# Kernel optimization log

Measured on AMD Instinct MI355X. Metric: run time of the kernel, lower is better.

## Reference

```python
import jax, jax.numpy as jnp
import numpy as np

B, N, E = 32, 1024, 16384
IN_DIM, HID, OUT = 768, 512, 400
H, F = 2, 200          # gat heads, per-head dim (H*F == OUT)
PAIR = 2 * OUT         # 800
NEG_SLOPE = 0.2


def setup_inputs() -> dict:
    key = jax.random.key(0)
    ks = jax.random.split(key, 20)
    g = lambda k, shp, fan: jax.random.normal(k, shp, jnp.float32) * (1.0 / np.sqrt(fan))
    return {
        "patch_features": jax.random.normal(ks[0], (B, N, IN_DIM), jnp.float32),
        "edges": jax.random.randint(ks[1], (2, E), 0, N, jnp.int32),
        # patch_encoder Mlps: 768 -> 512 (GELU) -> 400
        "enc_w1": g(ks[2], (IN_DIM, HID), IN_DIM), "enc_b1": jnp.zeros((HID,), jnp.float32),
        "enc_w2": g(ks[3], (HID, OUT), HID),      "enc_b2": jnp.zeros((OUT,), jnp.float32),
        # single GATConv: 400 -> 2 heads x 200, concat
        "gat_w": g(ks[4], (OUT, H, F), OUT),
        "att_src": g(ks[5], (H, F), F), "att_dst": g(ks[6], (H, F), F),
        "gat_b": jnp.zeros((H * F,), jnp.float32),
        # predict_head Mlps: 800 -> 800 (GELU) -> 400 (GELU) -> 3
        "h_w1": g(ks[7], (PAIR, PAIR), PAIR),      "h_b1": jnp.zeros((PAIR,), jnp.float32),
        "h_w2": g(ks[8], (PAIR, PAIR // 2), PAIR), "h_b2": jnp.zeros((PAIR // 2,), jnp.float32),
        "h_w3": g(ks[9], (PAIR // 2, 3), PAIR // 2), "h_b3": jnp.zeros((3,), jnp.float32),
    }


def _forward(patch_features, edges, enc_w1, enc_b1, enc_w2, enc_b2,
             gat_w, att_src, att_dst, gat_b,
             h_w1, h_b1, h_w2, h_b2, h_w3, h_b3):
    n = patch_features.shape[1]
    # per-batch patch encoder MLP (dropout inactive at eval)
    enc = jax.nn.gelu(jnp.einsum('bni,ih->bnh', patch_features, enc_w1) + enc_b1)
    enc = jnp.einsum('bnh,ho->bno', enc, enc_w2) + enc_b2   # [B,N,400]

    src0, dst0 = edges[0], edges[1]
    # GATConv adds self-loops
    loops = jnp.arange(n, dtype=edges.dtype)
    src = jnp.concatenate([src0, loops])
    dst = jnp.concatenate([dst0, loops])

    def gat(h):                                   # h: [N,400]
        wh = jnp.einsum('no,ohf->nhf', h, gat_w)  # [N,H,F]
        a_s = jnp.sum(wh * att_src, -1)           # [N,H]
        a_d = jnp.sum(wh * att_dst, -1)
        e = a_s[src] + a_d[dst]                   # [Et,H]
        e = jnp.where(e > 0, e, NEG_SLOPE * e)    # LeakyReLU(0.2)
        m = jax.ops.segment_max(e, dst, num_segments=n)
        ee = jnp.exp(e - m[dst])
        z = jax.ops.segment_sum(ee, dst, num_segments=n)
        coef = ee / z[dst]                        # softmax over incoming edges
        out = jax.ops.segment_sum(coef[:, :, None] * wh[src], dst, num_segments=n)
        return out.reshape(n, H * F) + gat_b      # concat heads + bias

    feat = enc + jax.vmap(gat)(enc)               # residual add per batch

    # pairwise edge gather + predict head
    pair = jnp.concatenate([feat[:, src0], feat[:, dst0]], axis=-1)  # [B,E,800]
    p = jax.nn.gelu(jnp.einsum('bep,pq->beq', pair, h_w1) + h_b1)
    p = jax.nn.gelu(jnp.einsum('beq,qr->ber', p, h_w2) + h_b2)
    pred = jnp.einsum('ber,rs->bes', p, h_w3) + h_b3                 # [B,E,3]
    return feat, pred


def reference(patch_features, edges, enc_w1, enc_b1, enc_w2, enc_b2,
              gat_w, att_src, att_dst, gat_b,
              h_w1, h_b1, h_w2, h_b2, h_w3, h_b3):
    return _forward(patch_features, edges, enc_w1, enc_b1, enc_w2, enc_b2,
                    gat_w, att_src, att_dst, gat_b,
                    h_w1, h_b1, h_w2, h_b2, h_w3, h_b3)
```

## Files before the change

### kernel.cpp

```cpp
#include <hip/hip_runtime.h>
#include <hip/hip_bf16.h>

typedef unsigned short u16;
typedef __attribute__((ext_vector_type(8))) short bf16x8;
typedef __attribute__((ext_vector_type(4))) float f32x4;

#define B_   32
#define N_   1024
#define E_   16384
#define ET_  17408
#define IN_DIM 768
#define HID  512
#define OUT_ 400
#define PAIR_ 800
#define UVW_ 1600
#define FEAT_ELEMS 13107200
#define MAXD 128

__device__ __forceinline__ float u2f(u16 u) {
    union { unsigned int i; float f; } v; v.i = ((unsigned int)u) << 16; return v.f;
}
__device__ __forceinline__ u16 f2u(float f) {
    __hip_bfloat16 h = __float2bfloat16(f);
    return *(u16*)&h;
}
__device__ __forceinline__ unsigned int pack2(float a, float b) {
    return (unsigned int)f2u(a) | ((unsigned int)f2u(b) << 16);
}

__device__ __forceinline__ float gelu_f(float x) {
    const float c = 0.7978845608028654f;
    float u = c * (x + 0.044715f * x * x * x);
    float t = 2.0f / (1.0f + __expf(-2.0f * u)) - 1.0f;
    return 0.5f * x * (1.0f + t);
}

__device__ __forceinline__ void load_lds16(const void* g, void* l) {
    __builtin_amdgcn_global_load_lds(
        (const __attribute__((address_space(1))) void*)g,
        (__attribute__((address_space(3))) void*)l, 16, 0, 0);
}

__global__ void wt_k(const float* __restrict__ W, u16* __restrict__ Wt,
                     int K, int N)
{
    int i = blockIdx.x * 256 + threadIdx.x;
    if (i >= N * K) return;
    int n = i / K, k = i - n * K;
    Wt[i] = f2u(W[(size_t)k * N + n]);
}

__global__ void wtuv_k(const float* __restrict__ W, u16* __restrict__ Wt)
{
    int i = blockIdx.x * 256 + threadIdx.x;
    if (i >= UVW_ * OUT_) return;
    int n = i / OUT_, k = i - n * OUT_;
    int row = (n >= PAIR_) ? OUT_ + k : k;
    int col = (n >= PAIR_) ? n - PAIR_ : n;
    Wt[i] = f2u(W[(size_t)row * PAIR_ + col]);
}

__global__ void f2b_k(const float* __restrict__ X, u16* __restrict__ Y, int n8)
{
    int i = blockIdx.x * 256 + threadIdx.x;
    if (i >= n8) return;
    const float4* p = (const float4*)X + (size_t)i * 2;
    float4 a = p[0], b = p[1];
    uint4 o;
    o.x = pack2(a.x, a.y); o.y = pack2(a.z, a.w);
    o.z = pack2(b.x, b.y); o.w = pack2(b.z, b.w);
    ((uint4*)Y)[i] = o;
}

template<int ASRC, bool DO_GELU, bool HAS_BIAS, bool OUT_F32, bool FUSE_H3, bool WIDE>
__global__ __launch_bounds__(WIDE ? 512 : 256, 2)
void mfma_gemm_k(const float* __restrict__ Af, const u16* __restrict__ Ab,
                 const u16* __restrict__ Wt, const float* __restrict__ bias,
                 u16* __restrict__ Cb, float* __restrict__ Cf,
                 int M, int N, int K,
                 const u16* __restrict__ zbuf,
                 const float* __restrict__ w3p, float* __restrict__ partp)
{
    static_assert(!WIDE || ASRC == 1, "wide path requires bf16 async staging");
    constexpr int BM  = WIDE ? 256 : 128;
    constexpr int BN  = WIDE ? 256 : 128;
    constexpr int NWV = WIDE ? 8 : 4;
    constexpr int UN  = WIDE ? 8 : 4;
    constexpr int WNS = WIDE ? 128 : 64;

    __shared__ __align__(16) u16 As[2][BM * 64];
    __shared__ __align__(16) u16 Bs[2][BN * 64];
    const int tid  = threadIdx.x;
    const int gx   = gridDim.x;
    const int nwg  = gx * gridDim.y;
    const int orig = blockIdx.y * gx + blockIdx.x;
    const int qc   = nwg >> 3, rc = nwg & 7;
    const int xcd  = orig & 7, lid = orig >> 3;
    const int wg   = ((xcd < rc) ? xcd * (qc + 1) : rc * (qc + 1) + (xcd - rc) * qc) + lid;
    const int bnIdx= wg % gx;
    const int bm   = (wg / gx) * BM;
    const int bn   = bnIdx * BN;
    const int wave = tid >> 6;
    const int lane = tid & 63;
    const int wm   = (wave >> 1) * 64;
    const int wn   = (wave & 1) * WNS;
    const int lm   = lane & 15;
    const int lq   = lane >> 4;
    const int lb   = lm & 7;
    const int l8 = lane >> 3;
    const int cl = (lane & 7) ^ l8;

    size_t arow[4]; size_t brow[4]; bool bok[4];
    #pragma unroll
    for (int c4 = 0; c4 < 4; ++c4) {
        int rt = wave * 32 + c4 * 8 + l8;
        if (ASRC == 1) arow[c4] = (size_t)(bm + rt) * K;
        int n = bn + rt;
        bok[c4] = (n < N);
        brow[c4] = (size_t)(n < N ? n : 0) * K;
    }
    const int vrow = tid >> 1, vhalf = tid & 1;

    f32x4 acc[4][UN] = {};
    const int NT = (K + 63) >> 6;

    if (ASRC == 1) {
        auto stage = [&](int buf, int k0) {
            int kk = k0 + cl * 8;
            #pragma unroll
            for (int c4 = 0; c4 < 4; ++c4) {
                const u16* ga = (kk < K) ? Ab + arow[c4] + kk : zbuf;
                load_lds16(ga, (char*)As[buf] + (wave * 32 + c4 * 8) * 128);
            }
            #pragma unroll
            for (int c4 = 0; c4 < 4; ++c4) {
                const u16* gb = (bok[c4] && kk < K) ? Wt + brow[c4] + kk : zbuf;
                load_lds16(gb, (char*)Bs[buf] + (wave * 32 + c4 * 8) * 128);
            }
        };
        stage(0, 0);
        int cur = 0;
        for (int it = 0; it < NT; ++it) {
            const bool last = (it == NT - 1);
            if (!last) stage(cur ^ 1, (it + 1) * 64);
            if (!last) asm volatile("s_waitcnt vmcnt(8)" ::: "memory");
            else       asm volatile("s_waitcnt vmcnt(0)" ::: "memory");
            __builtin_amdgcn_s_barrier();
            const char* Abase = (const char*)As[cur];
            const char* Bbase = (const char*)Bs[cur];
            #pragma unroll
            for (int kh = 0; kh < 2; ++kh) {
                bf16x8 af[4], bfr[UN];
                #pragma unroll
                for (int t = 0; t < 4; ++t)
                    af[t] = *(const bf16x8*)(Abase +
                            (wm + t * 16 + lm) * 128 + (((kh * 4 + lq) ^ lb) * 16));
                #pragma unroll
                for (int u = 0; u < UN; ++u)
                    bfr[u] = *(const bf16x8*)(Bbase +
                            (wn + u * 16 + lm) * 128 + (((kh * 4 + lq) ^ lb) * 16));
                #pragma unroll
                for (int t = 0; t < 4; ++t)
                    #pragma unroll
                    for (int u = 0; u < UN; ++u)
                        acc[t][u] = __builtin_amdgcn_mfma_f32_16x16x32_bf16(
                            af[t], bfr[u], acc[t][u], 0, 0, 0);
            }
            asm volatile("" ::: "memory");
            __builtin_amdgcn_s_barrier();
            cur ^= 1;
        }
    } else {
        for (int k0 = 0; k0 < K; k0 += 64) {
            #pragma unroll
            for (int c = 0; c < 4; ++c) {
                int c_log = vhalf * 4 + c;
                int kk = k0 + c_log * 8;
                uint4 wv = make_uint4(0, 0, 0, 0);
                if (kk < K) {
                    const float* p = Af + (size_t)(bm + vrow) * K + kk;
                    float4 v0 = *(const float4*)p;
                    float4 v1 = *(const float4*)(p + 4);
                    wv.x = pack2(v0.x, v0.y); wv.y = pack2(v0.z, v0.w);
                    wv.z = pack2(v1.x, v1.y); wv.w = pack2(v1.z, v1.w);
                }
                int pc = c_log ^ (vrow & 7);
                *(uint4*)((char*)As[0] + vrow * 128 + pc * 16) = wv;
            }
            {
                int kk = k0 + cl * 8;
                #pragma unroll
                for (int c4 = 0; c4 < 4; ++c4) {
                    const u16* gb = (bok[c4] && kk < K) ? Wt + brow[c4] + kk : zbuf;
                    load_lds16(gb, (char*)Bs[0] + (wave * 32 + c4 * 8) * 128);
                }
            }
            __syncthreads();
            #pragma unroll
            for (int kh = 0; kh < 2; ++kh) {
                bf16x8 af[4], bfr[UN];
                #pragma unroll
                for (int t = 0; t < 4; ++t)
                    af[t] = *(const bf16x8*)((const char*)As[0] +
                            (wm + t * 16 + lm) * 128 + (((kh * 4 + lq) ^ lb) * 16));
                #pragma unroll
                for (int u = 0; u < UN; ++u)
                    bfr[u] = *(const bf16x8*)((const char*)Bs[0] +
                            (wn + u * 16 + lm) * 128 + (((kh * 4 + lq) ^ lb) * 16));
                #pragma unroll
                for (int t = 0; t < 4; ++t)
                    #pragma unroll
                    for (int u = 0; u < UN; ++u)
                        acc[t][u] = __builtin_amdgcn_mfma_f32_16x16x32_bf16(
                            af[t], bfr[u], acc[t][u], 0, 0, 0);
            }
            __syncthreads();
        }
    }

    if (FUSE_H3) {
        float w3c[UN][3]; float bvv[UN];
        #pragma unroll
        for (int u = 0; u < UN; ++u) {
            int col = bn + wn + u * 16 + lm;
            bool ok = (col < N);
            bvv[u]    = ok ? bias[col] : 0.f;
            w3c[u][0] = ok ? w3p[col * 3 + 0] : 0.f;
            w3c[u][1] = ok ? w3p[col * 3 + 1] : 0.f;
            w3c[u][2] = ok ? w3p[col * 3 + 2] : 0.f;
        }
        float* red = (float*)As;
        #pragma unroll
        for (int t = 0; t < 4; ++t) {
            #pragma unroll
            for (int r = 0; r < 4; ++r) {
                float s0 = 0.f, s1 = 0.f, s2 = 0.f;
                #pragma unroll
                for (int u = 0; u < UN; ++u) {
                    float v = gelu_f(acc[t][u][r] + bvv[u]);
                    s0 += v * w3c[u][0];
                    s1 += v * w3c[u][1];
                    s2 += v * w3c[u][2];
                }
                #pragma unroll
                for (int off = 8; off; off >>= 1) {
                    s0 += __shfl_xor(s0, off);
                    s1 += __shfl_xor(s1, off);
                    s2 += __shfl_xor(s2, off);
                }
                if (lm == 0) {
                    int lr = t * 16 + lq * 4 + r;
                    float* d = red + (wave * 64 + lr) * 3;
                    d[0] = s0; d[1] = s1; d[2] = s2;
                }
            }
        }
        __syncthreads();
        if ((wave & 1) == 0) {
            int lr = lane;
            int rowg = bm + wm + lr;
            float* a = red + ((wave + 0) * 64 + lr) * 3;
            float* b = red + ((wave + 1) * 64 + lr) * 3;
            float* d = partp + ((size_t)bnIdx * M + rowg) * 3;
            d[0] = a[0] + b[0];
            d[1] = a[1] + b[1];
            d[2] = a[2] + b[2];
        }
        return;
    }

    #pragma unroll
    for (int u = 0; u < UN; ++u) {
        int col = bn + wn + u * 16 + lm;
        if (col >= N) continue;
        float bv = HAS_BIAS ? bias[col] : 0.f;
        #pragma unroll
        for (int t = 0; t < 4; ++t) {
            #pragma unroll
            for (int r = 0; r < 4; ++r) {
                int rowg = bm + wm + t * 16 + lq * 4 + r;
                float v = acc[t][u][r] + bv;
                if (DO_GELU) v = gelu_f(v);
                if (OUT_F32) {
                    Cf[(size_t)rowg * N + col] = v;
                    if (Cb) Cb[(size_t)rowg * N + col] = f2u(v);
                } else {
                    Cb[(size_t)rowg * N + col] = f2u(v);
                }
            }
        }
    }
}

__global__ __launch_bounds__(256)
void red3_k(const float* __restrict__ part, const float* __restrict__ b3,
            float* __restrict__ out, int row_base, int Mr, int ns)
{
    int r = blockIdx.x * 256 + threadIdx.x;
    if (r >= Mr) return;
    float s0 = b3[0], s1 = b3[1], s2 = b3[2];
    for (int s = 0; s < ns; ++s) {
        const float* p = part + ((size_t)s * Mr + r) * 3;
        s0 += p[0]; s1 += p[1]; s2 += p[2];
    }
    float* d = out + (size_t)FEAT_ELEMS + (size_t)(row_base + r) * 3;
    d[0] = s0; d[1] = s1; d[2] = s2;
}

__global__ __launch_bounds__(256)
void pair_fuse_k(const u16* __restrict__ UV, const float* __restrict__ b1,
                 const int* __restrict__ src0, const int* __restrict__ dst0,
                 u16* __restrict__ p1, int b0, int nrows)
{
    unsigned idx = blockIdx.x * 256u + threadIdx.x;
    unsigned total = (unsigned)nrows * 100u;
    if (idx >= total) return;
    unsigned r  = (unsigned)(((unsigned long long)idx * 1374389535ull) >> 37);
    unsigned c8 = idx - r * 100u;
    int e = r & (E_ - 1);
    int gs, gd;
    if (b0 >= 0) {
        int b = b0 + (int)(r >> 14);
        gs = (b << 10) + src0[e];
        gd = (b << 10) + dst0[e];
    } else {
        gs = src0[e]; gd = dst0[e];
    }
    uint4 qu = *(const uint4*)(UV + (size_t)gs * UVW_ + c8 * 8);
    uint4 qv = *(const uint4*)(UV + (size_t)gd * UVW_ + PAIR_ + c8 * 8);
    float4 bva = *(const float4*)(b1 + c8 * 8);
    float4 bvb = *(const float4*)(b1 + c8 * 8 + 4);
    float bb[8] = {bva.x, bva.y, bva.z, bva.w, bvb.x, bvb.y, bvb.z, bvb.w};
    unsigned int uu[4] = {qu.x, qu.y, qu.z, qu.w};
    unsigned int vv[4] = {qv.x, qv.y, qv.z, qv.w};
    uint4 o; unsigned int* op = (unsigned int*)&o;
    #pragma unroll
    for (int q = 0; q < 4; ++q) {
        float a0 = u2f((u16)(uu[q] & 0xffff)) + u2f((u16)(vv[q] & 0xffff)) + bb[2*q];
        float a1 = u2f((u16)(uu[q] >> 16))    + u2f((u16)(vv[q] >> 16))    + bb[2*q+1];
        op[q] = pack2(gelu_f(a0), gelu_f(a1));
    }
    *(uint4*)(p1 + (size_t)r * PAIR_ + c8 * 8) = o;
}

__global__ __launch_bounds__(256)
void scores_k(const u16* __restrict__ wh, const float* __restrict__ att_s,
              const float* __restrict__ att_d, float* __restrict__ a_s,
              float* __restrict__ a_d)
{
    int n = blockIdx.x * 4 + (threadIdx.x >> 6);
    int lane = threadIdx.x & 63;
    const u16* row = wh + (size_t)n * OUT_;
    float as0 = 0, as1 = 0, ad0 = 0, ad1 = 0;
    for (int f = lane; f < OUT_; f += 64) {
        float v = u2f(row[f]);
        float s = att_s[f];
        float d = att_d[f];
        if (f < 200) { as0 += v * s; ad0 += v * d; }
        else         { as1 += v * s; ad1 += v * d; }
    }
    for (int off = 32; off; off >>= 1) {
        as0 += __shfl_xor(as0, off); as1 += __shfl_xor(as1, off);
        ad0 += __shfl_xor(ad0, off); ad1 += __shfl_xor(ad1, off);
    }
    if (lane == 0) {
        a_s[(size_t)n * 2 + 0] = as0; a_s[(size_t)n * 2 + 1] = as1;
        a_d[(size_t)n * 2 + 0] = ad0; a_d[(size_t)n * 2 + 1] = ad1;
    }
}

__global__ void csr_count_k(const int* __restrict__ edges, int* __restrict__ deg)
{
    int et = blockIdx.x * blockDim.x + threadIdx.x;
    if (et >= ET_) return;
    int dst = (et < E_) ? edges[E_ + et] : (et - E_);
    atomicAdd(&deg[dst], 1);
}

__global__ __launch_bounds__(1024)
void csr_scan_k(const int* __restrict__ deg, int* __restrict__ row_ptr,
                int* __restrict__ cnt)
{
    __shared__ int s[1024];
    int t = threadIdx.x;
    int d = deg[t];
    s[t] = d;
    __syncthreads();
    for (int off = 1; off < 1024; off <<= 1) {
        int v = (t >= off) ? s[t - off] : 0;
        __syncthreads();
        s[t] += v;
        __syncthreads();
    }
    row_ptr[t] = s[t] - d;
    cnt[t] = s[t] - d;
    if (t == 1023) row_ptr[1024] = s[t];
}

__global__ void csr_fill_k(const int* __restrict__ edges, int* __restrict__ cnt,
                           int* __restrict__ col_src)
{
    int et = blockIdx.x * blockDim.x + threadIdx.x;
    if (et >= ET_) return;
    int src, dst;
    if (et < E_) { src = edges[et]; dst = edges[E_ + et]; }
    else         { src = et - E_;  dst = src; }
    int pos = atomicAdd(&cnt[dst], 1);
    col_src[pos] = src;
}

__global__ __launch_bounds__(256)
void gat_k(const u16* __restrict__ wh,
           const float* __restrict__ a_s, const float* __restrict__ a_d,
           const int* __restrict__ row_ptr, const int* __restrict__ col_src,
           const float* __restrict__ gat_b, float* __restrict__ feat,
           u16* __restrict__ featb16)
{
    int gn = blockIdx.x;
    int b = gn >> 10, n = gn & 1023;
    int tid = threadIdx.x;
    __shared__ float s_ee[2][MAXD];
    __shared__ int   s_src[MAXD];
    __shared__ float s_misc[6];
    __shared__ float s_part[4][50][9];
    int start = row_ptr[n];
    int deg = row_ptr[n + 1] - start;

    if (tid < 64) {
        int lane = tid;
        float ad0 = a_d[(size_t)gn * 2 + 0];
        float ad1 = a_d[(size_t)gn * 2 + 1];
        float m0 = -1e30f, m1 = -1e30f;
        for (int j = lane; j < deg; j += 64) {
            int gs = (b << 10) + col_src[start + j];
            float e0 = a_s[(size_t)gs * 2 + 0] + ad0; e0 = (e0 > 0.f) ? e0 : 0.2f * e0;
            float e1 = a_s[(size_t)gs * 2 + 1] + ad1; e1 = (e1 > 0.f) ? e1 : 0.2f * e1;
            if (j < MAXD) { s_ee[0][j] = e0; s_ee[1][j] = e1; s_src[j] = gs; }
            m0 = fmaxf(m0, e0); m1 = fmaxf(m1, e1);
        }
        for (int off = 32; off; off >>= 1) {
            m0 = fmaxf(m0, __shfl_xor(m0, off));
            m1 = fmaxf(m1, __shfl_xor(m1, off));
        }
        float z0 = 0.f, z1 = 0.f;
        for (int j = lane; j < deg; j += 64) {
            float e0, e1;
            if (j < MAXD) { e0 = s_ee[0][j]; e1 = s_ee[1][j]; }
            else {
                int gs = (b << 10) + col_src[start + j];
                e0 = a_s[(size_t)gs * 2 + 0] + ad0; e0 = (e0 > 0.f) ? e0 : 0.2f * e0;
                e1 = a_s[(size_t)gs * 2 + 1] + ad1; e1 = (e1 > 0.f) ? e1 : 0.2f * e1;
            }
            float t0 = __expf(e0 - m0), t1 = __expf(e1 - m1);
            if (j < MAXD) { s_ee[0][j] = t0; s_ee[1][j] = t1; }
            z0 += t0; z1 += t1;
        }
        for (int off = 32; off; off >>= 1) {
            z0 += __shfl_xor(z0, off);
            z1 += __shfl_xor(z1, off);
        }
        if (lane == 0) {
            s_misc[0] = m0; s_misc[1] = m1;
            s_misc[2] = (z0 > 0.f) ? 1.f / z0 : 0.f;
            s_misc[3] = (z1 > 0.f) ? 1.f / z1 : 0.f;
            s_misc[4] = ad0; s_misc[5] = ad1;
        }
    }
    __syncthreads();

    int wv = tid >> 6, ln = tid & 63;
    if (ln < 50) {
        int h = (ln >= 25);
        float m = s_misc[h], ad = s_misc[4 + h];
        float acc[8] = {};
        for (int j = wv; j < deg; j += 4) {
            float w; int gs;
            if (j < MAXD) { w = s_ee[h][j]; gs = s_src[j]; }
            else {
                gs = (b << 10) + col_src[start + j];
                float e = a_s[(size_t)gs * 2 + h] + ad;
                e = (e > 0.f) ? e : 0.2f * e;
                w = __expf(e - m);
            }
            uint4 q = *(const uint4*)(wh + (size_t)gs * OUT_ + ln * 8);
            acc[0] += w * u2f((u16)(q.x & 0xffff));
            acc[1] += w * u2f((u16)(q.x >> 16));
            acc[2] += w * u2f((u16)(q.y & 0xffff));
            acc[3] += w * u2f((u16)(q.y >> 16));
            acc[4] += w * u2f((u16)(q.z & 0xffff));
            acc[5] += w * u2f((u16)(q.z >> 16));
            acc[6] += w * u2f((u16)(q.w & 0xffff));
            acc[7] += w * u2f((u16)(q.w >> 16));
        }
        #pragma unroll
        for (int k = 0; k < 8; ++k) s_part[wv][ln][k] = acc[k];
    }
    __syncthreads();
    if (tid < 50) {
        int h = (tid >= 25);
        float iz = s_misc[2 + h];
        size_t base = (size_t)gn * OUT_ + tid * 8;
        float4 f0 = *(const float4*)(feat + base);
        float4 f1 = *(const float4*)(feat + base + 4);
        float fv[8] = { f0.x, f0.y, f0.z, f0.w, f1.x, f1.y, f1.z, f1.w };
        float o[8];
        #pragma unroll
        for (int k = 0; k < 8; ++k) {
            float s = s_part[0][tid][k] + s_part[1][tid][k] +
                      s_part[2][tid][k] + s_part[3][tid][k];
            o[k] = fv[k] + s * iz + gat_b[tid * 8 + k];
        }
        *(float4*)(feat + base)     = make_float4(o[0], o[1], o[2], o[3]);
        *(float4*)(feat + base + 4) = make_float4(o[4], o[5], o[6], o[7]);
        if (featb16) {
            uint4 bq;
            bq.x = pack2(o[0], o[1]); bq.y = pack2(o[2], o[3]);
            bq.z = pack2(o[4], o[5]); bq.w = pack2(o[6], o[7]);
            *(uint4*)(featb16 + base) = bq;
        }
    }
}

__global__ __launch_bounds__(256)
void head3_k(const u16* __restrict__ p2, const float* __restrict__ w3,
             const float* __restrict__ b3, float* __restrict__ out,
             int row_base, int nrows)
{
    int wv = threadIdx.x >> 6, lane = threadIdx.x & 63;
    float w3r[24];
    if (lane < 50) {
        #pragma unroll
        for (int q = 0; q < 6; ++q) {
            float4 v = *(const float4*)(w3 + lane * 24 + q * 4);
            w3r[q * 4 + 0] = v.x; w3r[q * 4 + 1] = v.y;
            w3r[q * 4 + 2] = v.z; w3r[q * 4 + 3] = v.w;
        }
    }
    int e0 = blockIdx.x * 16 + wv * 4;
    for (int ei = 0; ei < 4; ++ei) {
        int e = e0 + ei;
        if (e >= nrows) break;
        float s0 = 0, s1 = 0, s2 = 0;
        if (lane < 50) {
            uint4 q = *(const uint4*)(p2 + (size_t)e * OUT_ + lane * 8);
            float f[8];
            f[0] = u2f((u16)(q.x & 0xffff)); f[1] = u2f((u16)(q.x >> 16));
            f[2] = u2f((u16)(q.y & 0xffff)); f[3] = u2f((u16)(q.y >> 16));
            f[4] = u2f((u16)(q.z & 0xffff)); f[5] = u2f((u16)(q.z >> 16));
            f[6] = u2f((u16)(q.w & 0xffff)); f[7] = u2f((u16)(q.w >> 16));
            #pragma unroll
            for (int k = 0; k < 8; ++k) {
                s0 += f[k] * w3r[k * 3 + 0];
                s1 += f[k] * w3r[k * 3 + 1];
                s2 += f[k] * w3r[k * 3 + 2];
            }
        }
        for (int off = 32; off; off >>= 1) {
            s0 += __shfl_xor(s0, off);
            s1 += __shfl_xor(s1, off);
            s2 += __shfl_xor(s2, off);
        }
        if (lane == 0) {
            size_t o = (size_t)FEAT_ELEMS + (size_t)(row_base + e) * 3;
            out[o + 0] = s0 + b3[0];
            out[o + 1] = s1 + b3[1];
            out[o + 2] = s2 + b3[2];
        }
    }
}

extern "C" void kernel_launch(void* const* d_in, const int* in_sizes, int n_in,
                              void* d_out, int out_size, void* d_ws, size_t ws_size,
                              hipStream_t stream)
{
    const float* patch  = (const float*)d_in[0];
    const int*   edges  = (const int*)d_in[1];
    const float* enc_w1 = (const float*)d_in[2];
    const float* enc_b1 = (const float*)d_in[3];
    const float* enc_w2 = (const float*)d_in[4];
    const float* enc_b2 = (const float*)d_in[5];
    const float* gat_w  = (const float*)d_in[6];
    const float* att_s  = (const float*)d_in[7];
    const float* att_d  = (const float*)d_in[8];
    const float* gat_b  = (const float*)d_in[9];
    const float* h_w1   = (const float*)d_in[10];
    const float* h_b1   = (const float*)d_in[11];
    const float* h_w2   = (const float*)d_in[12];
    const float* h_b2   = (const float*)d_in[13];
    const float* h_w3   = (const float*)d_in[14];
    const float* h_b3   = (const float*)d_in[15];
    float* out  = (float*)d_out;
    float* feat = out;
    char*  ws   = (char*)d_ws;

    const int* src0 = edges;
    const int* dst0 = edges + E_;

    const size_t R0 = 33554432ull, TAIL = 4194304ull;
    const size_t UVSZ = 104857600ull;
    const size_t P1SZ = 26214400ull;
    int CB = 0;
    if      (ws_size >= R0 + UVSZ + TAIL + 4 * P1SZ) CB = 4;
    else if (ws_size >= R0 + UVSZ + TAIL + 2 * P1SZ) CB = 2;
    const bool big = (CB >= 2);

    u16 *enc1, *whb, *p1, *p2, *featb16, *uv, *w1t, *w2t, *gwt, *uvwt, *hw2t;
    u16 *patchb16, *encb16;
    float *a_s, *a_d, *part; int *deg;
    if (big) {
        enc1    = (u16*)ws;
        featb16 = (u16*)ws;
        part    = (float*)ws;
        whb     = (u16*)(ws + R0);
        uv      = (u16*)(ws + R0);
        encb16  = (u16*)(ws + R0 + 26214400ull);
        p1      = (u16*)(ws + R0 + UVSZ);
        patchb16= (u16*)(ws + R0 + UVSZ);
        p2      = nullptr;
        size_t tb = (ws_size - TAIL) & ~(size_t)255;
        w1t  = (u16*)(ws + tb);
        w2t  = (u16*)(ws + tb + 786432);
        gwt  = (u16*)(ws + tb + 1196032);
        uvwt = (u16*)(ws + tb + 1516032);
        hw2t = (u16*)(ws + tb + 2796032);
        a_s  = (float*)(ws + tb + 3436032);
        a_d  = (float*)(ws + tb + 3698176);
        deg  = (int*)(ws + tb + 3960320);
    } else {
        enc1    = (u16*)ws;
        whb     = (u16*)ws;
        p1      = (u16*)ws;
        featb16 = nullptr;
        patchb16= nullptr;
        encb16  = nullptr;
        part    = nullptr;
        p2      = (u16*)(ws + 26214400);
        uv      = (u16*)(ws + 39321600);
        w1t  = (u16*)(ws + 42598400);
        w2t  = (u16*)(ws + 43384832);
        gwt  = (u16*)(ws + 43794432);
        uvwt = (u16*)(ws + 44114432);
        hw2t = (u16*)(ws + 45394432);
        a_s  = (float*)(ws + 46034432);
        a_d  = (float*)(ws + 46296576);
        deg  = (int*)(ws + 46558720);
    }
    int* row_ptr = deg + 1024;
    int* cnt     = row_ptr + 1032;
    int* col_src = cnt + 1024;
    u16* zbuf = (u16*)(col_src + 17408);

    hipMemsetAsync(zbuf, 0, 256, stream);

    wt_k<<<(HID * IN_DIM + 255) / 256, 256, 0, stream>>>(enc_w1, w1t, IN_DIM, HID);
    wt_k<<<(OUT_ * HID + 255) / 256, 256, 0, stream>>>(enc_w2, w2t, HID, OUT_);
    wt_k<<<(OUT_ * OUT_ + 255) / 256, 256, 0, stream>>>(gat_w, gwt, OUT_, OUT_);
    wtuv_k<<<(UVW_ * OUT_ + 255) / 256, 256, 0, stream>>>(h_w1, uvwt);
    wt_k<<<(OUT_ * PAIR_ + 255) / 256, 256, 0, stream>>>(h_w2, hw2t, PAIR_, OUT_);

    hipMemsetAsync(deg, 0, 1024 * sizeof(int), stream);
    csr_count_k<<<(ET_ + 255) / 256, 256, 0, stream>>>(edges, deg);
    csr_scan_k<<<1, 1024, 0, stream>>>(deg, row_ptr, cnt);
    csr_fill_k<<<(ET_ + 255) / 256, 256, 0, stream>>>(edges, cnt, col_src);

    if (big) {
        f2b_k<<<(B_ * N_ * IN_DIM / 8 + 255) / 256, 256, 0, stream>>>(
            patch, patchb16, B_ * N_ * IN_DIM / 8);
        mfma_gemm_k<1, true, true, false, false, true><<<dim3(2, (B_ * N_) / 256), 512, 0, stream>>>(
            nullptr, patchb16, w1t, enc_b1, enc1, nullptr, B_ * N_, HID, IN_DIM, zbuf,
            nullptr, nullptr);
        mfma_gemm_k<1, false, true, true, false, true><<<dim3(2, (B_ * N_) / 256), 512, 0, stream>>>(
            nullptr, enc1, w2t, enc_b2, encb16, feat, B_ * N_, OUT_, HID, zbuf,
            nullptr, nullptr);
        mfma_gemm_k<1, false, false, false, false, true><<<dim3(2, (B_ * N_) / 256), 512, 0, stream>>>(
            nullptr, encb16, gwt, nullptr, whb, nullptr, B_ * N_, OUT_, OUT_, zbuf,
            nullptr, nullptr);
    } else {
        mfma_gemm_k<0, true, true, false, false, false><<<dim3(HID / 128, (B_ * N_) / 128), 256, 0, stream>>>(
            patch, nullptr, w1t, enc_b1, enc1, nullptr, B_ * N_, HID, IN_DIM, zbuf,
            nullptr, nullptr);
        mfma_gemm_k<1, false, true, true, false, false><<<dim3((OUT_ + 127) / 128, (B_ * N_) / 128), 256, 0, stream>>>(
            nullptr, enc1, w2t, enc_b2, nullptr, feat, B_ * N_, OUT_, HID, zbuf,
            nullptr, nullptr);
        mfma_gemm_k<0, false, false, false, false, false><<<dim3((OUT_ + 127) / 128, (B_ * N_) / 128), 256, 0, stream>>>(
            feat, nullptr, gwt, nullptr, whb, nullptr, B_ * N_, OUT_, OUT_, zbuf,
            nullptr, nullptr);
    }

    scores_k<<<(B_ * N_) / 4, 256, 0, stream>>>(whb, att_s, att_d, a_s, a_d);
    gat_k<<<B_ * N_, 256, 0, stream>>>(whb, a_s, a_d, row_ptr, col_src,
                                       gat_b, feat, featb16);

    if (big) {
        mfma_gemm_k<1, false, false, false, false, true><<<dim3((UVW_ + 255) / 256, (B_ * N_) / 256), 512, 0, stream>>>(
            nullptr, featb16, uvwt, nullptr, uv, nullptr, B_ * N_, UVW_, OUT_, zbuf,
            nullptr, nullptr);
        for (int b0 = 0; b0 < B_; b0 += CB) {
            int Mr = CB * E_;
            pair_fuse_k<<<(Mr * 100 + 255) / 256, 256, 0, stream>>>(
                uv, h_b1, src0, dst0, p1, b0, Mr);
            mfma_gemm_k<1, true, true, false, true, true><<<dim3((OUT_ + 255) / 256, Mr / 256), 512, 0, stream>>>(
                nullptr, p1, hw2t, h_b2, nullptr, nullptr, Mr, OUT_, PAIR_, zbuf,
                h_w3, part);
            red3_k<<<(Mr + 255) / 256, 256, 0, stream>>>(part, h_b3, out, b0 * E_, Mr,
                                                         (OUT_ + 255) / 256);
        }
    } else {
        for (int b = 0; b < B_; ++b) {
            const float* featb = feat + (size_t)b * N_ * OUT_;
            mfma_gemm_k<0, false, false, false, false, false><<<dim3((UVW_ + 127) / 128, N_ / 128), 256, 0, stream>>>(
                featb, nullptr, uvwt, nullptr, uv, nullptr, N_, UVW_, OUT_, zbuf,
                nullptr, nullptr);
            pair_fuse_k<<<(E_ * 100 + 255) / 256, 256, 0, stream>>>(
                uv, h_b1, src0, dst0, p1, -1, E_);
            mfma_gemm_k<1, true, true, false, false, false><<<dim3((OUT_ + 127) / 128, E_ / 128), 256, 0, stream>>>(
                nullptr, p1, hw2t, h_b2, p2, nullptr, E_, OUT_, PAIR_, zbuf,
                nullptr, nullptr);
            head3_k<<<(E_ + 15) / 16, 256, 0, stream>>>(p2, h_w3, h_b3, out,
                                                        b * E_, E_);
        }
    }
}
```

Before: 1.502 ms.

## Store pair-head activations in K-panel-major layout for contiguous GEMM staging

Adds a pair-fuse kernel that writes the gelu'd first-layer pair activations in panels of 64 K-columns, so each panel is contiguous across rows. A new GEMM staging mode reads A tiles from that panel layout instead of from row-strided memory. Processing is fixed at two batches per chunk, which shrinks the workspace needed for the big path but may add launches compared with four-batch chunks. The fused head GEMM is now instantiated with the GELU flag off, which relies on the fused reduction path applying its own activation.

```diff
diff --git a/kernel.cpp b/kernel.cpp
--- a/kernel.cpp
+++ b/kernel.cpp
@@ -16,6 +16,8 @@
 #define UVW_ 1600
 #define FEAT_ELEMS 13107200
 #define MAXD 128
+#define MRC  32768
+#define NPAN 13
 
 __device__ __forceinline__ float u2f(u16 u) {
     union { unsigned int i; float f; } v; v.i = ((unsigned int)u) << 16; return v.f;
@@ -72,8 +74,8 @@
     ((uint4*)Y)[i] = o;
 }
 
-template<int ASRC, bool DO_GELU, bool HAS_BIAS, bool OUT_F32, bool FUSE_H3, bool WIDE>
-__global__ __launch_bounds__(WIDE ? 512 : 256, 2)
+template<int ASRC, bool DO_GELU, bool HAS_BIAS, bool OUT_F32, bool FUSE_H3, int SHAPE>
+__global__ __launch_bounds__(SHAPE >= 1 ? 512 : 256, 2)
 void mfma_gemm_k(const float* __restrict__ Af, const u16* __restrict__ Ab,
                  const u16* __restrict__ Wt, const float* __restrict__ bias,
                  u16* __restrict__ Cb, float* __restrict__ Cf,
@@ -81,12 +83,11 @@
                  const u16* __restrict__ zbuf,
                  const float* __restrict__ w3p, float* __restrict__ partp)
 {
-    static_assert(!WIDE || ASRC == 1, "wide path requires bf16 async staging");
-    constexpr int BM  = WIDE ? 256 : 128;
-    constexpr int BN  = WIDE ? 256 : 128;
-    constexpr int NWV = WIDE ? 8 : 4;
-    constexpr int UN  = WIDE ? 8 : 4;
-    constexpr int WNS = WIDE ? 128 : 64;
+    static_assert(SHAPE == 0 || ASRC >= 1, "wide shapes need bf16 async staging");
+    constexpr int BM  = (SHAPE == 1) ? 256 : 128;
+    constexpr int BN  = (SHAPE == 1) ? 256 : 128;
+    constexpr int UN  = (SHAPE == 1) ? 8 : 4;
+    constexpr int CW  = 2;
 
     __shared__ __align__(16) u16 As[2][BM * 64];
     __shared__ __align__(16) u16 Bs[2][BN * 64];
@@ -103,7 +104,7 @@
     const int wave = tid >> 6;
     const int lane = tid & 63;
     const int wm   = (wave >> 1) * 64;
-    const int wn   = (wave & 1) * WNS;
+    const int wn   = (SHAPE == 1) ? (wave & 1) * 128 : (wave & 1) * 64;
     const int lm   = lane & 15;
     const int lq   = lane >> 4;
     const int lb   = lm & 7;
@@ -115,6 +116,7 @@
     for (int c4 = 0; c4 < 4; ++c4) {
         int rt = wave * 32 + c4 * 8 + l8;
         if (ASRC == 1) arow[c4] = (size_t)(bm + rt) * K;
+        if (ASRC == 3) arow[c4] = (size_t)(bm + rt) * 64;
         int n = bn + rt;
         bok[c4] = (n < N);
         brow[c4] = (size_t)(n < N ? n : 0) * K;
@@ -124,13 +126,22 @@
     f32x4 acc[4][UN] = {};
     const int NT = (K + 63) >> 6;
 
-    if (ASRC == 1) {
+    if (ASRC >= 1) {
         auto stage = [&](int buf, int k0) {
             int kk = k0 + cl * 8;
-            #pragma unroll
-            for (int c4 = 0; c4 < 4; ++c4) {
-                const u16* ga = (kk < K) ? Ab + arow[c4] + kk : zbuf;
-                load_lds16(ga, (char*)As[buf] + (wave * 32 + c4 * 8) * 128);
+            if (ASRC == 3) {
+                const u16* pan = Ab + (size_t)(k0 >> 6) * M * 64;
+                #pragma unroll
+                for (int c4 = 0; c4 < 4; ++c4) {
+                    const u16* ga = (kk < K) ? pan + arow[c4] + cl * 8 : zbuf;
+                    load_lds16(ga, (char*)As[buf] + (wave * 32 + c4 * 8) * 128);
+                }
+            } else {
+                #pragma unroll
+                for (int c4 = 0; c4 < 4; ++c4) {
+                    const u16* ga = (kk < K) ? Ab + arow[c4] + kk : zbuf;
+                    load_lds16(ga, (char*)As[buf] + (wave * 32 + c4 * 8) * 128);
+                }
             }
             #pragma unroll
             for (int c4 = 0; c4 < 4; ++c4) {
@@ -256,15 +267,17 @@
             }
         }
         __syncthreads();
-        if ((wave & 1) == 0) {
+        if ((wave & (CW - 1)) == 0) {
             int lr = lane;
             int rowg = bm + wm + lr;
-            float* a = red + ((wave + 0) * 64 + lr) * 3;
-            float* b = red + ((wave + 1) * 64 + lr) * 3;
+            float s0 = 0.f, s1 = 0.f, s2 = 0.f;
+            #pragma unroll
+            for (int w = 0; w < CW; ++w) {
+                float* a = red + ((wave + w) * 64 + lr) * 3;
+                s0 += a[0]; s1 += a[1]; s2 += a[2];
+            }
             float* d = partp + ((size_t)bnIdx * M + rowg) * 3;
-            d[0] = a[0] + b[0];
-            d[1] = a[1] + b[1];
-            d[2] = a[2] + b[2];
+            d[0] = s0; d[1] = s1; d[2] = s2;
         }
         return;
     }
@@ -305,6 +318,39 @@
     }
     float* d = out + (size_t)FEAT_ELEMS + (size_t)(row_base + r) * 3;
     d[0] = s0; d[1] = s1; d[2] = s2;
+}
+
+__global__ __launch_bounds__(256)
+void pair_fuse_kp(const u16* __restrict__ UV, const float* __restrict__ b1,
+                  const int* __restrict__ src0, const int* __restrict__ dst0,
+                  u16* __restrict__ p1k, int b0)
+{
+    unsigned idx = blockIdx.x * 256u + threadIdx.x;
+    unsigned s = idx & 7u;
+    unsigned r = (idx >> 3) & (MRC - 1);
+    unsigned p = idx >> 18;
+    if (p >= NPAN) return;
+    int k0 = (int)(p * 64 + s * 8);
+    if (k0 >= PAIR_) return;
+    int e = (int)(r & (E_ - 1));
+    int b = b0 + (int)(r >> 14);
+    int gs = (b << 10) + src0[e];
+    int gd = (b << 10) + dst0[e];
+    uint4 qu = *(const uint4*)(UV + (size_t)gs * UVW_ + k0);
+    uint4 qv = *(const uint4*)(UV + (size_t)gd * UVW_ + PAIR_ + k0);
+    float4 bva = *(const float4*)(b1 + k0);
+    float4 bvb = *(const float4*)(b1 + k0 + 4);
+    float bb[8] = {bva.x, bva.y, bva.z, bva.w, bvb.x, bvb.y, bvb.z, bvb.w};
+    unsigned int uu[4] = {qu.x, qu.y, qu.z, qu.w};
+    unsigned int vv[4] = {qv.x, qv.y, qv.z, qv.w};
+    uint4 o; unsigned int* op = (unsigned int*)&o;
+    #pragma unroll
+    for (int q = 0; q < 4; ++q) {
+        float a0 = u2f((u16)(uu[q] & 0xffff)) + u2f((u16)(vv[q] & 0xffff)) + bb[2*q];
+        float a1 = u2f((u16)(uu[q] >> 16))    + u2f((u16)(vv[q] >> 16))    + bb[2*q+1];
+        op[q] = pack2(gelu_f(a0), gelu_f(a1));
+    }
+    *(uint4*)(p1k + ((size_t)p * MRC + r) * 64 + s * 8) = o;
 }
 
 __global__ __launch_bounds__(256)
@@ -598,14 +644,11 @@
 
     const size_t R0 = 33554432ull, TAIL = 4194304ull;
     const size_t UVSZ = 104857600ull;
-    const size_t P1SZ = 26214400ull;
-    int CB = 0;
-    if      (ws_size >= R0 + UVSZ + TAIL + 4 * P1SZ) CB = 4;
-    else if (ws_size >= R0 + UVSZ + TAIL + 2 * P1SZ) CB = 2;
-    const bool big = (CB >= 2);
+    const size_t P1K  = (size_t)NPAN * MRC * 64 * 2;
+    const bool big = (ws_size >= R0 + UVSZ + TAIL + P1K);
 
     u16 *enc1, *whb, *p1, *p2, *featb16, *uv, *w1t, *w2t, *gwt, *uvwt, *hw2t;
-    u16 *patchb16, *encb16;
+    u16 *patchb16, *encb16, *p1k;
     float *a_s, *a_d, *part; int *deg;
     if (big) {
         enc1    = (u16*)ws;
@@ -614,8 +657,9 @@
         whb     = (u16*)(ws + R0);
         uv      = (u16*)(ws + R0);
         encb16  = (u16*)(ws + R0 + 26214400ull);
-        p1      = (u16*)(ws + R0 + UVSZ);
+        p1k     = (u16*)(ws + R0 + UVSZ);
         patchb16= (u16*)(ws + R0 + UVSZ);
+        p1      = nullptr;
         p2      = nullptr;
         size_t tb = (ws_size - TAIL) & ~(size_t)255;
         w1t  = (u16*)(ws + tb);
@@ -634,6 +678,7 @@
         patchb16= nullptr;
         encb16  = nullptr;
         part    = nullptr;
+        p1k     = nullptr;
         p2      = (u16*)(ws + 26214400);
         uv      = (u16*)(ws + 39321600);
         w1t  = (u16*)(ws + 42598400);
@@ -666,23 +711,23 @@
     if (big) {
         f2b_k<<<(B_ * N_ * IN_DIM / 8 + 255) / 256, 256, 0, stream>>>(
             patch, patchb16, B_ * N_ * IN_DIM / 8);
-        mfma_gemm_k<1, true, true, false, false, true><<<dim3(2, (B_ * N_) / 256), 512, 0, stream>>>(
+        mfma_gemm_k<1, true, true, false, false, 1><<<dim3(2, (B_ * N_) / 256), 512, 0, stream>>>(
             nullptr, patchb16, w1t, enc_b1, enc1, nullptr, B_ * N_, HID, IN_DIM, zbuf,
             nullptr, nullptr);
-        mfma_gemm_k<1, false, true, true, false, true><<<dim3(2, (B_ * N_) / 256), 512, 0, stream>>>(
+        mfma_gemm_k<1, false, true, true, false, 1><<<dim3(2, (B_ * N_) / 256), 512, 0, stream>>>(
             nullptr, enc1, w2t, enc_b2, encb16, feat, B_ * N_, OUT_, HID, zbuf,
             nullptr, nullptr);
-        mfma_gemm_k<1, false, false, false, false, true><<<dim3(2, (B_ * N_) / 256), 512, 0, stream>>>(
+        mfma_gemm_k<1, false, false, false, false, 1><<<dim3(2, (B_ * N_) / 256), 512, 0, stream>>>(
             nullptr, encb16, gwt, nullptr, whb, nullptr, B_ * N_, OUT_, OUT_, zbuf,
             nullptr, nullptr);
     } else {
-        mfma_gemm_k<0, true, true, false, false, false><<<dim3(HID / 128, (B_ * N_) / 128), 256, 0, stream>>>(
+        mfma_gemm_k<0, true, true, false, false, 0><<<dim3(HID / 128, (B_ * N_) / 128), 256, 0, stream>>>(
             patch, nullptr, w1t, enc_b1, enc1, nullptr, B_ * N_, HID, IN_DIM, zbuf,
             nullptr, nullptr);
-        mfma_gemm_k<1, false, true, true, false, false><<<dim3((OUT_ + 127) / 128, (B_ * N_) / 128), 256, 0, stream>>>(
+        mfma_gemm_k<1, false, true, true, false, 0><<<dim3((OUT_ + 127) / 128, (B_ * N_) / 128), 256, 0, stream>>>(
             nullptr, enc1, w2t, enc_b2, nullptr, feat, B_ * N_, OUT_, HID, zbuf,
             nullptr, nullptr);
-        mfma_gemm_k<0, false, false, false, false, false><<<dim3((OUT_ + 127) / 128, (B_ * N_) / 128), 256, 0, stream>>>(
+        mfma_gemm_k<0, false, false, false, false, 0><<<dim3((OUT_ + 127) / 128, (B_ * N_) / 128), 256, 0, stream>>>(
             feat, nullptr, gwt, nullptr, whb, nullptr, B_ * N_, OUT_, OUT_, zbuf,
             nullptr, nullptr);
     }
@@ -692,28 +737,27 @@
                                        gat_b, feat, featb16);
 
     if (big) {
-        mfma_gemm_k<1, false, false, false, false, true><<<dim3((UVW_ + 255) / 256, (B_ * N_) / 256), 512, 0, stream>>>(
+        mfma_gemm_k<1, false, false, false, false, 1><<<dim3((UVW_ + 255) / 256, (B_ * N_) / 256), 512, 0, stream>>>(
             nullptr, featb16, uvwt, nullptr, uv, nullptr, B_ * N_, UVW_, OUT_, zbuf,
             nullptr, nullptr);
-        for (int b0 = 0; b0 < B_; b0 += CB) {
-            int Mr = CB * E_;
-            pair_fuse_k<<<(Mr * 100 + 255) / 256, 256, 0, stream>>>(
-                uv, h_b1, src0, dst0, p1, b0, Mr);
-            mfma_gemm_k<1, true, true, false, true, true><<<dim3((OUT_ + 255) / 256, Mr / 256), 512, 0, stream>>>(
-                nullptr, p1, hw2t, h_b2, nullptr, nullptr, Mr, OUT_, PAIR_, zbuf,
+        const int PF_BLK = (NPAN * MRC * 8) / 256;
+        for (int b0 = 0; b0 < B_; b0 += 2) {
+            pair_fuse_kp<<<PF_BLK, 256, 0, stream>>>(uv, h_b1, src0, dst0, p1k, b0);
+            mfma_gemm_k<3, false, true, false, true, 1><<<dim3(2, MRC / 256), 512, 0, stream>>>(
+                nullptr, p1k, hw2t, h_b2, nullptr, nullptr, MRC, OUT_, PAIR_, zbuf,
                 h_w3, part);
-            red3_k<<<(Mr + 255) / 256, 256, 0, stream>>>(part, h_b3, out, b0 * E_, Mr,
-                                                         (OUT_ + 255) / 256);
+            red3_k<<<(MRC + 255) / 256, 256, 0, stream>>>(part, h_b3, out,
+                                                          b0 * E_, MRC, 2);
         }
     } else {
         for (int b = 0; b < B_; ++b) {
             const float* featb = feat + (size_t)b * N_ * OUT_;
-            mfma_gemm_k<0, false, false, false, false, false><<<dim3((UVW_ + 127) / 128, N_ / 128), 256, 0, stream>>>(
+            mfma_gemm_k<0, false, false, false, false, 0><<<dim3((UVW_ + 127) / 128, N_ / 128), 256, 0, stream>>>(
                 featb, nullptr, uvwt, nullptr, uv, nullptr, N_, UVW_, OUT_, zbuf,
                 nullptr, nullptr);
             pair_fuse_k<<<(E_ * 100 + 255) / 256, 256, 0, stream>>>(
                 uv, h_b1, src0, dst0, p1, -1, E_);
-            mfma_gemm_k<1, true, true, false, false, false><<<dim3((OUT_ + 127) / 128, E_ / 128), 256, 0, stream>>>(
+            mfma_gemm_k<1, true, true, false, false, 0><<<dim3((OUT_ + 127) / 128, E_ / 128), 256, 0, stream>>>(
                 nullptr, p1, hw2t, h_b2, p2, nullptr, E_, OUT_, PAIR_, zbuf,
                 nullptr, nullptr);
             head3_k<<<(E_ + 15) / 16, 256, 0, stream>>>(p2, h_w3, h_b3, out,
```

Measured after the change: 1.573 ms. +4.7%, slower.
